# Performance work log

Measured on AMD Instinct MI355X. Metric: run time of the kernel, lower is better.

The kernel has to match this reference:

```python
import jax, jax.numpy as jnp
import numpy as np

NUM_GRAPHS = 512


def setup_inputs() -> dict:
    key = jax.random.key(0)
    ks = jax.random.split(key, 16)
    N, E = 50000, 800000
    x = jax.random.normal(ks[0], (N, 3), dtype=jnp.float32)
    edge_index = jax.random.randint(ks[1], (2, E), 0, N, dtype=jnp.int64)
    batch = jnp.sort(jax.random.randint(ks[2], (N,), 0, NUM_GRAPHS, dtype=jnp.int64))

    def glorot(k, shape):
        fan_in, fan_out = shape
        lim = (6.0 / (fan_in + fan_out)) ** 0.5
        return jax.random.uniform(k, shape, jnp.float32, -lim, lim)

    return {
        "x": x, "edge_index": edge_index, "batch": batch,
        "W1": glorot(ks[3], (3, 32)),   "b1": jnp.zeros((32,), jnp.float32),
        "W2": glorot(ks[4], (32, 64)),  "b2": jnp.zeros((64,), jnp.float32),
        "W3": glorot(ks[5], (64, 128)), "b3": jnp.zeros((128,), jnp.float32),
        "Wf1": glorot(ks[6], (128, 32)), "bf1": jnp.zeros((32,), jnp.float32),
        "Wf2": glorot(ks[7], (32, 4)),   "bf2": jnp.zeros((4,), jnp.float32),
    }


def _gcn_conv(x, src, dst, norm, W, b, N):
    # GCNConv: h = x W, then symmetric-normalized aggregation, then bias.
    h = x @ W                                   # [N, out]
    msg = h[src] * norm[:, None]                # [E+N, out] gathered edge messages
    out = jax.ops.segment_sum(msg, dst, num_segments=N)
    return out + b


def reference(x, edge_index, batch, W1, b1, W2, b2, W3, b3, Wf1, bf1, Wf2, bf2):
    N = x.shape[0]
    loops = jnp.arange(N, dtype=edge_index.dtype)
    src = jnp.concatenate([edge_index[0], loops])   # add self-loops (GCNConv default)
    dst = jnp.concatenate([edge_index[1], loops])
    # symmetric normalization deg^-1/2[src] * deg^-1/2[dst], deg counted on dst
    deg = jax.ops.segment_sum(jnp.ones_like(dst, dtype=x.dtype), dst, num_segments=N)
    dinv = jnp.where(deg > 0, jax.lax.rsqrt(deg), 0.0)
    norm = dinv[src] * dinv[dst]                    # [E+N]

    h = jax.nn.relu(_gcn_conv(x, src, dst, norm, W1, b1, N))
    h = jax.nn.relu(_gcn_conv(h, src, dst, norm, W2, b2, N))
    h = jax.nn.relu(_gcn_conv(h, src, dst, norm, W3, b3, N))

    # global mean pool over graphs
    sums = jax.ops.segment_sum(h, batch, num_segments=NUM_GRAPHS)
    cnts = jax.ops.segment_sum(jnp.ones((N,), h.dtype), batch, num_segments=NUM_GRAPHS)
    pooled = sums / jnp.maximum(cnts, 1.0)[:, None]   # [G, 128]

    z = jax.nn.relu(pooled @ Wf1 + bf1)
    return z @ Wf2 + bf2                              # [G, 4]
```

## Files before the change

### kernel.cpp

```cpp
#include <hip/hip_runtime.h>

#define NN 50000
#define NE 800000
#define NG 512
#define CAP 64
#define NP 196
#define CH 3200
#define NCH 250

__global__ __launch_bounds__(256) void p1_hist_k(const int* __restrict__ dst,
                                                 int* __restrict__ Ht, int e) {
    __shared__ int lh[NP];
    int t = threadIdx.x, b = blockIdx.x;
    if (t < NP) lh[t] = 0;
    __syncthreads();
    int i0 = b * CH, i1 = min(e, i0 + CH);
    for (int i = i0 + t; i < i1; i += 256) atomicAdd(&lh[dst[i] >> 8], 1);
    __syncthreads();
    if (t < NP) Ht[t * NCH + b] = lh[t];
}

__global__ __launch_bounds__(256) void p2a_k(int* __restrict__ Ht, int* __restrict__ tot) {
    __shared__ int sh[256];
    int p = blockIdx.x, t = threadIdx.x;
    int v = (t < NCH) ? Ht[p * NCH + t] : 0;
    sh[t] = v;
    __syncthreads();
    for (int off = 1; off < 256; off <<= 1) {
        int x = (t >= off) ? sh[t - off] : 0;
        __syncthreads();
        sh[t] += x;
        __syncthreads();
    }
    if (t < NCH) Ht[p * NCH + t] = sh[t] - v;
    if (t == 255) tot[p] = sh[255];
}

__global__ __launch_bounds__(256) void p2b_k(const int* __restrict__ tot,
                                             int* __restrict__ start) {
    __shared__ int sh[256];
    int t = threadIdx.x;
    int v = (t < NP) ? tot[t] : 0;
    sh[t] = v;
    __syncthreads();
    for (int off = 1; off < 256; off <<= 1) {
        int x = (t >= off) ? sh[t - off] : 0;
        __syncthreads();
        sh[t] += x;
        __syncthreads();
    }
    if (t < NP) start[t] = sh[t] - v;
    if (t == 255) start[NP] = sh[255];
}

__global__ __launch_bounds__(256) void p3_place_k(const int* __restrict__ src,
                                                  const int* __restrict__ dst,
                                                  const int* __restrict__ Ht,
                                                  const int* __restrict__ start,
                                                  int* __restrict__ pak, int e) {
    __shared__ int cur[NP];
    int t = threadIdx.x, b = blockIdx.x;
    if (t < NP) cur[t] = start[t] + Ht[t * NCH + b];
    __syncthreads();
    int i0 = b * CH, i1 = min(e, i0 + CH);
    for (int i = i0 + t; i < i1; i += 256) {
        int d = dst[i], s = src[i];
        int p = d >> 8, dl = d & 255;
        int pos = atomicAdd(&cur[p], 1);
        pak[pos] = s | (dl << 16);
    }
}

__global__ __launch_bounds__(256) void p4_build_k(const int* __restrict__ pak,
                                                   const int* __restrict__ start,
                                                   const float* __restrict__ x,
                                                   int* __restrict__ fill,
                                                   float* __restrict__ dinv,
                                                   float* __restrict__ xs,
                                                   int* __restrict__ eidx, int n) {
    __shared__ int lh[256], curn[256];
    int p = blockIdx.x, t = threadIdx.x;
    lh[t] = 0;
    curn[t] = 0;
    __syncthreads();
    int s0 = start[p], s1 = start[p + 1];
    for (int i = s0 + t; i < s1; i += 256) atomicAdd(&lh[pak[i] >> 16], 1);
    __syncthreads();
    int node = p * 256 + t;
    if (node < n) {
        int dg = lh[t];
        fill[node] = dg;
        float d = rsqrtf((float)(dg + 1));
        dinv[node] = d;
        float4 v;
        v.x = x[node * 3 + 0] * d;
        v.y = x[node * 3 + 1] * d;
        v.z = x[node * 3 + 2] * d;
        v.w = 0.0f;
        *(float4*)(xs + (size_t)node * 4) = v;
    }
    __syncthreads();
    for (int i = s0 + t; i < s1; i += 256) {
        int w = pak[i];
        int dl = w >> 16, s = w & 0xFFFF;
        int pos = atomicAdd(&curn[dl], 1) & (CAP - 1);
        eidx[(size_t)(p * 256 + dl) * CAP + pos] = s;
    }
}

__global__ __launch_bounds__(256) void fused_l1_k(
    const int* __restrict__ deg, const int* __restrict__ eidx,
    const float* __restrict__ xs, const float* __restrict__ W1,
    const float* __restrict__ b1, const float* __restrict__ dinv,
    float* __restrict__ A2, int n) {
    __shared__ float act[64][4];
    int t = threadIdx.x;
    int node0 = blockIdx.x * 64;
    {
        int node = node0 + (t >> 2);
        int f = t & 3;
        if (node < n) {
            int e1 = deg[node];
            const int* __restrict__ eb = eidx + node * CAP;
            float acc = xs[(size_t)node * 4 + f];
            int e = 0;
            for (; e + 4 <= e1; e += 4) {
                int4 s = *(const int4*)(eb + e);
                float v0 = xs[(size_t)s.x * 4 + f];
                float v1 = xs[(size_t)s.y * 4 + f];
                float v2 = xs[(size_t)s.z * 4 + f];
                float v3 = xs[(size_t)s.w * 4 + f];
                acc += (v0 + v1) + (v2 + v3);
            }
            for (; e < e1; ++e) acc += xs[(size_t)eb[e] * 4 + f];
            act[t >> 2][f] = acc;
        }
    }
    __syncthreads();
    int f = t & 31;
    int nl0 = t >> 5;
#pragma unroll
    for (int i = 0; i < 8; ++i) {
        int nl = nl0 + i * 8;
        int node = node0 + nl;
        if (node < n) {
            float acc = act[nl][0] * W1[f] + act[nl][1] * W1[32 + f] + act[nl][2] * W1[64 + f];
            float s = dinv[node];
            A2[(size_t)node * 32 + f] = fmaxf(fmaf(s, acc, b1[f]), 0.0f) * s;
        }
    }
}

template <int F>
__global__ __launch_bounds__(256) void gather4_k(const int* __restrict__ deg,
                                                 const int* __restrict__ eidx,
                                                 const float* __restrict__ A,
                                                 float* __restrict__ B, int n) {
    constexpr int FV = F / 4;
    constexpr int NPB = 256 / FV;
    int t = threadIdx.x;
    int node = blockIdx.x * NPB + t / FV;
    int j = (t % FV) * 4;
    if (node >= n) return;
    int e1 = deg[node];
    const int* __restrict__ eb = eidx + node * CAP;
    const float* __restrict__ Aj = A + j;
    float4 a0 = *(const float4*)(Aj + (size_t)node * F);
    float4 a1 = make_float4(0.f, 0.f, 0.f, 0.f);
    int e = 0;
    for (; e + 8 <= e1; e += 8) {
        int4 sa = *(const int4*)(eb + e);
        int4 sb = *(const int4*)(eb + e + 4);
        float4 v0 = *(const float4*)(Aj + (size_t)sa.x * F);
        float4 v1 = *(const float4*)(Aj + (size_t)sa.y * F);
        float4 v2 = *(const float4*)(Aj + (size_t)sa.z * F);
        float4 v3 = *(const float4*)(Aj + (size_t)sa.w * F);
        float4 v4 = *(const float4*)(Aj + (size_t)sb.x * F);
        float4 v5 = *(const float4*)(Aj + (size_t)sb.y * F);
        float4 v6 = *(const float4*)(Aj + (size_t)sb.z * F);
        float4 v7 = *(const float4*)(Aj + (size_t)sb.w * F);
        a0.x += (v0.x + v1.x) + (v2.x + v3.x);
        a0.y += (v0.y + v1.y) + (v2.y + v3.y);
        a0.z += (v0.z + v1.z) + (v2.z + v3.z);
        a0.w += (v0.w + v1.w) + (v2.w + v3.w);
        a1.x += (v4.x + v5.x) + (v6.x + v7.x);
        a1.y += (v4.y + v5.y) + (v6.y + v7.y);
        a1.z += (v4.z + v5.z) + (v6.z + v7.z);
        a1.w += (v4.w + v5.w) + (v6.w + v7.w);
    }
    for (; e < e1; ++e) {
        float4 v = *(const float4*)(Aj + (size_t)eb[e] * F);
        a0.x += v.x; a0.y += v.y; a0.z += v.z; a0.w += v.w;
    }
    a0.x += a1.x; a0.y += a1.y; a0.z += a1.z; a0.w += a1.w;
    *(float4*)(B + (size_t)node * F + j) = a0;
}

template <int Fin, int Fout, int NPB, bool SCALE_OUT>
__global__ __launch_bounds__(256) void mmB_k(
    const float* __restrict__ G, const float* __restrict__ W,
    const float* __restrict__ bias, const float* __restrict__ dinv,
    float* __restrict__ Aout, int n) {
    constexpr int FL = Fout / 4;
    constexpr int NGRP = 256 / FL;
    constexpr int NPT = NPB / NGRP;
    __shared__ float act[NPB][Fin];
    int t = threadIdx.x;
    int node0 = blockIdx.x * NPB;
    constexpr int TOT4 = NPB * Fin / 4;
    const float4* __restrict__ G4 = (const float4*)(G + (size_t)node0 * Fin);
    float4* act4 = (float4*)&act[0][0];
    for (int i = t; i < TOT4; i += 256) {
        int nl = i / (Fin / 4);
        float4 v = make_float4(0.f, 0.f, 0.f, 0.f);
        if (node0 + nl < n) v = G4[i];
        act4[i] = v;
    }
    __syncthreads();
    int f4 = (t % FL) * 4;
    int nlbase = (t / FL) * NPT;
    float4 acc[NPT];
#pragma unroll
    for (int i = 0; i < NPT; ++i) acc[i] = make_float4(0.f, 0.f, 0.f, 0.f);
    for (int k = 0; k < Fin; k += 4) {
        float4 a[NPT];
#pragma unroll
        for (int i = 0; i < NPT; ++i) a[i] = *(const float4*)&act[nlbase + i][k];
#pragma unroll
        for (int kk = 0; kk < 4; ++kk) {
            float4 w = *(const float4*)(W + (size_t)(k + kk) * Fout + f4);
#pragma unroll
            for (int i = 0; i < NPT; ++i) {
                float av = (&a[i].x)[kk];
                acc[i].x = fmaf(av, w.x, acc[i].x);
                acc[i].y = fmaf(av, w.y, acc[i].y);
                acc[i].z = fmaf(av, w.z, acc[i].z);
                acc[i].w = fmaf(av, w.w, acc[i].w);
            }
        }
    }
    float4 bv = *(const float4*)(bias + f4);
#pragma unroll
    for (int i = 0; i < NPT; ++i) {
        int node = node0 + nlbase + i;
        if (node < n) {
            float s = dinv[node];
            float4 o;
            o.x = fmaxf(fmaf(s, acc[i].x, bv.x), 0.0f);
            o.y = fmaxf(fmaf(s, acc[i].y, bv.y), 0.0f);
            o.z = fmaxf(fmaf(s, acc[i].z, bv.z), 0.0f);
            o.w = fmaxf(fmaf(s, acc[i].w, bv.w), 0.0f);
            if (SCALE_OUT) { o.x *= s; o.y *= s; o.z *= s; o.w *= s; }
            *(float4*)(Aout + (size_t)node * Fout + f4) = o;
        }
    }
}

#define NPB_POOL 32
__global__ __launch_bounds__(128) void pool2_k(
    const float* __restrict__ H, const int* __restrict__ batch,
    float* __restrict__ pooled, float* __restrict__ cntg, int n) {
    int f = threadIdx.x;
    int n0 = blockIdx.x * NPB_POOL;
    if (n0 >= n) return;
    int n1 = min(n0 + NPB_POOL, n);
    float acc = 0.0f, cct = 0.0f;
    int cur = batch[n0];
    for (int node = n0; node < n1; ++node) {
        int g = batch[node];
        if (g != cur) {
            atomicAdd(&pooled[cur * 128 + f], acc);
            if (f == 0) atomicAdd(&cntg[cur], cct);
            acc = 0.0f;
            cct = 0.0f;
            cur = g;
        }
        acc += H[(size_t)node * 128 + f];
        cct += 1.0f;
    }
    atomicAdd(&pooled[cur * 128 + f], acc);
    if (f == 0) atomicAdd(&cntg[cur], cct);
}

__global__ __launch_bounds__(64) void head_k(
    const float* __restrict__ pooled, const float* __restrict__ cnt,
    const float* __restrict__ Wf1, const float* __restrict__ bf1,
    const float* __restrict__ Wf2, const float* __restrict__ bf2,
    float* __restrict__ out) {
    __shared__ float pm[128];
    __shared__ float z[32];
    int g = blockIdx.x, t = threadIdx.x;
    float c = fmaxf(cnt[g], 1.0f);
    pm[t] = pooled[g * 128 + t] / c;
    pm[t + 64] = pooled[g * 128 + 64 + t] / c;
    __syncthreads();
    if (t < 32) {
        float acc = bf1[t];
#pragma unroll 4
        for (int k = 0; k < 128; ++k) acc = fmaf(pm[k], Wf1[k * 32 + t], acc);
        z[t] = fmaxf(acc, 0.0f);
    }
    __syncthreads();
    if (t < 4) {
        float acc = bf2[t];
#pragma unroll
        for (int j = 0; j < 32; ++j) acc = fmaf(z[j], Wf2[j * 4 + t], acc);
        out[g * 4 + t] = acc;
    }
}

extern "C" void kernel_launch(void* const* d_in, const int* in_sizes, int n_in,
                              void* d_out, int out_size, void* d_ws, size_t ws_size,
                              hipStream_t stream) {
    const float* x    = (const float*)d_in[0];
    const int*   ei   = (const int*)d_in[1];
    const int*   batch= (const int*)d_in[2];
    const float* W1   = (const float*)d_in[3];
    const float* b1   = (const float*)d_in[4];
    const float* W2   = (const float*)d_in[5];
    const float* b2   = (const float*)d_in[6];
    const float* W3   = (const float*)d_in[7];
    const float* b3   = (const float*)d_in[8];
    const float* Wf1  = (const float*)d_in[9];
    const float* bf1  = (const float*)d_in[10];
    const float* Wf2  = (const float*)d_in[11];
    const float* bf2  = (const float*)d_in[12];
    float* out = (float*)d_out;

    int*   fill   = (int*)d_ws;
    float* pooled = (float*)(fill + NN);
    float* cntg   = pooled + NG * 128;
    float* dinv   = cntg + NG;
    float* xs     = dinv + NN;
    float* A2     = xs + (size_t)NN * 4;
    float* A3     = A2 + (size_t)NN * 32;
    float* H3     = A3 + (size_t)NN * 64;
    float* G      = H3 + (size_t)NN * 128;
    int*   eidx   = (int*)(G + (size_t)NN * 64);

    int* pak   = (int*)G;
    int* Ht    = (int*)H3;
    int* tot   = Ht + NP * NCH;
    int* start = tot + 256;

    const int* src = ei;
    const int* dst = ei + NE;

    hipMemsetAsync(pooled, 0, (size_t)(NG * 128 + NG) * 4, stream);
    p1_hist_k<<<NCH, 256, 0, stream>>>(dst, Ht, NE);
    p2a_k<<<NP, 256, 0, stream>>>(Ht, tot);
    p2b_k<<<1, 256, 0, stream>>>(tot, start);
    p3_place_k<<<NCH, 256, 0, stream>>>(src, dst, Ht, start, pak, NE);
    p4_build_k<<<NP, 256, 0, stream>>>(pak, start, x, fill, dinv, xs, eidx, NN);

    fused_l1_k<<<(NN + 63) / 64, 256, 0, stream>>>(fill, eidx, xs, W1, b1, dinv, A2, NN);

    gather4_k<32><<<(NN + 31) / 32, 256, 0, stream>>>(fill, eidx, A2, G, NN);
    mmB_k<32, 64, 32, true><<<(NN + 31) / 32, 256, 0, stream>>>(G, W2, b2, dinv, A3, NN);

    gather4_k<64><<<(NN + 15) / 16, 256, 0, stream>>>(fill, eidx, A3, G, NN);
    mmB_k<64, 128, 32, false><<<(NN + 31) / 32, 256, 0, stream>>>(G, W3, b3, dinv, H3, NN);

    pool2_k<<<(NN + NPB_POOL - 1) / NPB_POOL, 128, 0, stream>>>(H3, batch, pooled, cntg, NN);
    head_k<<<NG, 64, 0, stream>>>(pooled, cntg, Wf1, bf1, Wf2, bf2, out);
}
```

Measured before the change: 225.4 us.

## Fuse mean-pool into head kernel via binary search, widen gather unroll to 16

Replaces the atomic-based pooling kernel, the memset and the separate head kernel with one kernel per graph. Each block binary-searches the sorted batch array for its node range, sums the rows directly and then runs the MLP head. This removes the atomics, the memset and one launch, but leaves only 512 blocks to read H3. The gather kernel also gets a 16-edge unrolled loop with four accumulators plus a 4-edge remainder loop, to keep more loads in flight at the cost of extra registers.

New measurement: 222.8 us, median of 2. About the same (-1.2%).

```diff
diff --git a/kernel.cpp b/kernel.cpp
--- a/kernel.cpp
+++ b/kernel.cpp
@@ -167,10 +167,14 @@
     const float* __restrict__ Aj = A + j;
     float4 a0 = *(const float4*)(Aj + (size_t)node * F);
     float4 a1 = make_float4(0.f, 0.f, 0.f, 0.f);
+    float4 a2 = make_float4(0.f, 0.f, 0.f, 0.f);
+    float4 a3 = make_float4(0.f, 0.f, 0.f, 0.f);
     int e = 0;
-    for (; e + 8 <= e1; e += 8) {
+    for (; e + 16 <= e1; e += 16) {
         int4 sa = *(const int4*)(eb + e);
         int4 sb = *(const int4*)(eb + e + 4);
+        int4 sc = *(const int4*)(eb + e + 8);
+        int4 sd = *(const int4*)(eb + e + 12);
         float4 v0 = *(const float4*)(Aj + (size_t)sa.x * F);
         float4 v1 = *(const float4*)(Aj + (size_t)sa.y * F);
         float4 v2 = *(const float4*)(Aj + (size_t)sa.z * F);
@@ -179,6 +183,14 @@
         float4 v5 = *(const float4*)(Aj + (size_t)sb.y * F);
         float4 v6 = *(const float4*)(Aj + (size_t)sb.z * F);
         float4 v7 = *(const float4*)(Aj + (size_t)sb.w * F);
+        float4 v8 = *(const float4*)(Aj + (size_t)sc.x * F);
+        float4 v9 = *(const float4*)(Aj + (size_t)sc.y * F);
+        float4 va = *(const float4*)(Aj + (size_t)sc.z * F);
+        float4 vb = *(const float4*)(Aj + (size_t)sc.w * F);
+        float4 vc = *(const float4*)(Aj + (size_t)sd.x * F);
+        float4 vd = *(const float4*)(Aj + (size_t)sd.y * F);
+        float4 ve = *(const float4*)(Aj + (size_t)sd.z * F);
+        float4 vf = *(const float4*)(Aj + (size_t)sd.w * F);
         a0.x += (v0.x + v1.x) + (v2.x + v3.x);
         a0.y += (v0.y + v1.y) + (v2.y + v3.y);
         a0.z += (v0.z + v1.z) + (v2.z + v3.z);
@@ -187,12 +199,34 @@
         a1.y += (v4.y + v5.y) + (v6.y + v7.y);
         a1.z += (v4.z + v5.z) + (v6.z + v7.z);
         a1.w += (v4.w + v5.w) + (v6.w + v7.w);
+        a2.x += (v8.x + v9.x) + (va.x + vb.x);
+        a2.y += (v8.y + v9.y) + (va.y + vb.y);
+        a2.z += (v8.z + v9.z) + (va.z + vb.z);
+        a2.w += (v8.w + v9.w) + (va.w + vb.w);
+        a3.x += (vc.x + vd.x) + (ve.x + vf.x);
+        a3.y += (vc.y + vd.y) + (ve.y + vf.y);
+        a3.z += (vc.z + vd.z) + (ve.z + vf.z);
+        a3.w += (vc.w + vd.w) + (ve.w + vf.w);
+    }
+    for (; e + 4 <= e1; e += 4) {
+        int4 sa = *(const int4*)(eb + e);
+        float4 v0 = *(const float4*)(Aj + (size_t)sa.x * F);
+        float4 v1 = *(const float4*)(Aj + (size_t)sa.y * F);
+        float4 v2 = *(const float4*)(Aj + (size_t)sa.z * F);
+        float4 v3 = *(const float4*)(Aj + (size_t)sa.w * F);
+        a1.x += (v0.x + v1.x) + (v2.x + v3.x);
+        a1.y += (v0.y + v1.y) + (v2.y + v3.y);
+        a1.z += (v0.z + v1.z) + (v2.z + v3.z);
+        a1.w += (v0.w + v1.w) + (v2.w + v3.w);
     }
     for (; e < e1; ++e) {
         float4 v = *(const float4*)(Aj + (size_t)eb[e] * F);
         a0.x += v.x; a0.y += v.y; a0.z += v.z; a0.w += v.w;
     }
-    a0.x += a1.x; a0.y += a1.y; a0.z += a1.z; a0.w += a1.w;
+    a0.x += (a1.x + a2.x) + a3.x;
+    a0.y += (a1.y + a2.y) + a3.y;
+    a0.z += (a1.z + a2.z) + a3.z;
+    a0.w += (a1.w + a2.w) + a3.w;
     *(float4*)(B + (size_t)node * F + j) = a0;
 }
 
@@ -256,43 +290,40 @@
     }
 }
 
-#define NPB_POOL 32
-__global__ __launch_bounds__(128) void pool2_k(
+__device__ __forceinline__ int lbound_d(const int* __restrict__ a, int n, int key) {
+    int lo = 0, hi = n;
+    while (lo < hi) {
+        int m = (lo + hi) >> 1;
+        if (a[m] < key) lo = m + 1; else hi = m;
+    }
+    return lo;
+}
+
+__global__ __launch_bounds__(128) void poolhead_k(
     const float* __restrict__ H, const int* __restrict__ batch,
-    float* __restrict__ pooled, float* __restrict__ cntg, int n) {
-    int f = threadIdx.x;
-    int n0 = blockIdx.x * NPB_POOL;
-    if (n0 >= n) return;
-    int n1 = min(n0 + NPB_POOL, n);
-    float acc = 0.0f, cct = 0.0f;
-    int cur = batch[n0];
-    for (int node = n0; node < n1; ++node) {
-        int g = batch[node];
-        if (g != cur) {
-            atomicAdd(&pooled[cur * 128 + f], acc);
-            if (f == 0) atomicAdd(&cntg[cur], cct);
-            acc = 0.0f;
-            cct = 0.0f;
-            cur = g;
-        }
-        acc += H[(size_t)node * 128 + f];
-        cct += 1.0f;
-    }
-    atomicAdd(&pooled[cur * 128 + f], acc);
-    if (f == 0) atomicAdd(&cntg[cur], cct);
-}
-
-__global__ __launch_bounds__(64) void head_k(
-    const float* __restrict__ pooled, const float* __restrict__ cnt,
     const float* __restrict__ Wf1, const float* __restrict__ bf1,
     const float* __restrict__ Wf2, const float* __restrict__ bf2,
-    float* __restrict__ out) {
+    float* __restrict__ out, int n) {
+    __shared__ int bnd[2];
     __shared__ float pm[128];
     __shared__ float z[32];
     int g = blockIdx.x, t = threadIdx.x;
-    float c = fmaxf(cnt[g], 1.0f);
-    pm[t] = pooled[g * 128 + t] / c;
-    pm[t + 64] = pooled[g * 128 + 64 + t] / c;
+    if (t == 0) bnd[0] = lbound_d(batch, n, g);
+    if (t == 1) bnd[1] = lbound_d(batch, n, g + 1);
+    __syncthreads();
+    int lo = bnd[0], hi = bnd[1];
+    float s0 = 0.f, s1 = 0.f, s2 = 0.f, s3 = 0.f;
+    int i = lo;
+    for (; i + 4 <= hi; i += 4) {
+        s0 += H[(size_t)i * 128 + t];
+        s1 += H[(size_t)(i + 1) * 128 + t];
+        s2 += H[(size_t)(i + 2) * 128 + t];
+        s3 += H[(size_t)(i + 3) * 128 + t];
+    }
+    for (; i < hi; ++i) s0 += H[(size_t)i * 128 + t];
+    float c = (float)(hi - lo);
+    c = fmaxf(c, 1.0f);
+    pm[t] = ((s0 + s1) + (s2 + s3)) / c;
     __syncthreads();
     if (t < 32) {
         float acc = bf1[t];
@@ -304,7 +335,7 @@
     if (t < 4) {
         float acc = bf2[t];
 #pragma unroll
-        for (int j = 0; j < 32; ++j) acc = fmaf(z[j], Wf2[j * 4 + t], acc);
+        for (int jj = 0; jj < 32; ++jj) acc = fmaf(z[jj], Wf2[jj * 4 + t], acc);
         out[g * 4 + t] = acc;
     }
 }
@@ -328,9 +359,7 @@
     float* out = (float*)d_out;
 
     int*   fill   = (int*)d_ws;
-    float* pooled = (float*)(fill + NN);
-    float* cntg   = pooled + NG * 128;
-    float* dinv   = cntg + NG;
+    float* dinv   = (float*)(fill + NN);
     float* xs     = dinv + NN;
     float* A2     = xs + (size_t)NN * 4;
     float* A3     = A2 + (size_t)NN * 32;
@@ -346,7 +375,6 @@
     const int* src = ei;
     const int* dst = ei + NE;
 
-    hipMemsetAsync(pooled, 0, (size_t)(NG * 128 + NG) * 4, stream);
     p1_hist_k<<<NCH, 256, 0, stream>>>(dst, Ht, NE);
     p2a_k<<<NP, 256, 0, stream>>>(Ht, tot);
     p2b_k<<<1, 256, 0, stream>>>(tot, start);
@@ -361,6 +389,5 @@
     gather4_k<64><<<(NN + 15) / 16, 256, 0, stream>>>(fill, eidx, A3, G, NN);
     mmB_k<64, 128, 32, false><<<(NN + 31) / 32, 256, 0, stream>>>(G, W3, b3, dinv, H3, NN);
 
-    pool2_k<<<(NN + NPB_POOL - 1) / NPB_POOL, 128, 0, stream>>>(H3, batch, pooled, cntg, NN);
-    head_k<<<NG, 64, 0, stream>>>(pooled, cntg, Wf1, bf1, Wf2, bf2, out);
-}
+    poolhead_k<<<NG, 128, 0, stream>>>(H3, batch, Wf1, bf1, Wf2, bf2, out, NN);
+}
```
